# Kernel tuning notes

Hardware: AMD Instinct MI355X
Metric: run time of the kernel (lower is better)

Reference implementation:

```python
import jax, jax.numpy as jnp
import numpy as np

B, S, D = 1, 2048, 1024
H, HD = 16, 64            # attn_num, head dim (D = H*HD)
TE, K, ED = 16, 2, 512    # experts, top_k, expert_dim
DS = 2048                 # shared_expert_dim
EPS = 1e-5
THETA = 10000.0
RSF = 1.0                 # routed_scaling_factor


def rmsnorm(x, w):
    return x * jax.lax.rsqrt(jnp.mean(x * x, axis=-1, keepdims=True) + EPS) * w


def rope(x):
    # x: [B,H,S,a]; half-split rotary as in RotaryEmb
    a = x.shape[-1]
    inv = (1.0 / THETA) ** (jnp.arange(0, a, 2, dtype=jnp.float32) / a)
    fr = jnp.outer(jnp.arange(x.shape[2], dtype=jnp.float32), inv)[None, None]  # [1,1,S,a/2]
    c, s = jnp.cos(fr), jnp.sin(fr)
    x1, x2 = jnp.split(x, 2, axis=-1)
    return jnp.concatenate([x1 * c + x2 * s, -x1 * s + x2 * c], axis=-1)


def setup_inputs() -> dict:
    key = jax.random.key(0)
    ks = jax.random.split(key, 16)
    w = 0.02
    return {
        "x_input": jax.random.normal(ks[0], (B, S, D), jnp.float32),
        "indices": jax.random.randint(ks[1], (B * S, K), 0, TE),
        "values": jax.random.normal(ks[2], (B * S, K), jnp.float32),
        "attn_w": jax.random.normal(ks[3], (3 * D, D), jnp.float32) * w,
        "attn_o_w": jax.random.normal(ks[4], (D, D), jnp.float32) * w,
        "attn_norm_w": jnp.ones((D,), jnp.float32),
        "ffn_norm_w": jnp.ones((D,), jnp.float32),
        "ffn_experts": jax.random.normal(ks[5], (3, TE, D, ED), jnp.float32) * w,
        "main_keys": jax.random.normal(ks[6], (D, TE), jnp.float32) * w,
        "main_bias": jnp.zeros((TE,), jnp.float32),
        "output_coeff": jnp.ones((1, 1, D), jnp.float32),
        "ffn_up_w": jax.random.normal(ks[7], (2 * DS, D), jnp.float32) * w,
        "ffn_down_w": jax.random.normal(ks[8], (D, DS), jnp.float32) * w,
        "shared_norm_w": jnp.ones((D,), jnp.float32),
    }


def reference(x_input, indices, values, attn_w, attn_o_w, attn_norm_w, ffn_norm_w,
              ffn_experts, main_keys, main_bias, output_coeff, ffn_up_w,
              ffn_down_w, shared_norm_w):
    # --- attention block ---
    x = rmsnorm(x_input, attn_norm_w)
    qkv = x @ attn_w.T                                  # [B,S,3D]
    xq, xk, xv = jnp.split(qkv, 3, axis=-1)
    def heads(t):
        return t.reshape(B, S, H, HD).transpose(0, 2, 1, 3)  # [B,H,S,HD]
    q, k, v = rope(heads(xq)), rope(heads(xk)), heads(xv)
    att = jnp.einsum('bhqa,bhka->bhqk', q, k) / jnp.sqrt(jnp.float32(HD))
    causal = jnp.tril(jnp.ones((S, S), bool))
    att = jnp.where(causal, att, jnp.finfo(att.dtype).min)
    att = jax.nn.softmax(att, axis=-1)
    o = jnp.einsum('bhqk,bhka->bhqa', att, v)
    x_attn = o.transpose(0, 2, 1, 3).reshape(B, S, D)
    x_ffn_input = x_attn @ attn_o_w.T + x_input

    # --- router ---
    x_ffn = rmsnorm(x_ffn_input, ffn_norm_w)
    T = B * S
    token_values = (x_ffn @ main_keys).reshape(T, TE)
    tv = jnp.take_along_axis(token_values, indices, axis=-1)  # [T,K]
    vals = values + tv + main_bias[indices]
    scores = jax.nn.softmax(vals, axis=-1) * RSF              # [T,K]

    # --- grouped GEMM experts (SwiGLU), dense combine over experts ---
    combine = jnp.zeros((T, TE), x_ffn.dtype).at[
        jnp.arange(T)[:, None], indices].add(scores)          # [T,TE]
    xf = x_ffn.reshape(T, D)
    h1 = jnp.einsum('td,edh->eth', xf, ffn_experts[0])
    h2 = jnp.einsum('td,edh->eth', xf, ffn_experts[1])
    g = jax.nn.silu(h1) * h2                                  # [TE,T,ED]
    ye = jnp.einsum('eth,edh->etd', g, ffn_experts[2])        # [TE,T,D]
    y = jnp.einsum('etd,te->td', ye, combine).reshape(B, S, D)
    y = y * output_coeff

    # --- shared SwiGLU expert ---
    x1, x2 = jnp.split(x_ffn @ ffn_up_w.T, 2, axis=-1)
    y_shared = (jax.nn.silu(x1) * x2) @ ffn_down_w.T
    y_shared = rmsnorm(y_shared, shared_norm_w)

    return y + y_shared + x_ffn_input
```

## Files before the change

### kernel.cpp

```cpp
#include <hip/hip_runtime.h>
#include <hip/hip_bf16.h>

using bf16 = __hip_bfloat16;

#define S_   2048
#define D_   1024
#define H_   16
#define HD_  64
#define TE_  16
#define ED_  512
#define DS_  2048
#define CAP_ 512

#define NEG_ -1e30f

typedef __attribute__((ext_vector_type(8))) short bf16x8;
typedef __attribute__((ext_vector_type(4))) short bf16x4;
typedef __attribute__((ext_vector_type(4))) float f32x4;
#define MFMA16(a, b, c) __builtin_amdgcn_mfma_f32_16x16x32_bf16(a, b, c, 0, 0, 0)

__device__ __forceinline__ void storeF(float* p, float v) { *p = v; }
__device__ __forceinline__ void storeF(bf16* p, float v)  { *p = __float2bfloat16(v); }
__device__ __forceinline__ short cvt1(float f) {
    bf16 h = __float2bfloat16(f);
    return *(short*)&h;
}
__device__ __forceinline__ float b2f(short s) {
    return __uint_as_float(((unsigned)(unsigned short)s) << 16);
}

__device__ __forceinline__ void load16(const bf16* g, short* l) {
    __builtin_amdgcn_global_load_lds(
        (const __attribute__((address_space(1))) unsigned*)g,
        (__attribute__((address_space(3))) unsigned*)l, 16, 0, 0);
}

__global__ __launch_bounds__(256) void convert_kernel(
        const float* __restrict__ src, bf16* __restrict__ dst)
{
    const size_t i = ((size_t)blockIdx.x*256 + threadIdx.x)*8;
    const float4 f0 = *(const float4*)(src + i);
    const float4 f1 = *(const float4*)(src + i + 4);
    short t8[8];
    t8[0]=cvt1(f0.x); t8[1]=cvt1(f0.y); t8[2]=cvt1(f0.z); t8[3]=cvt1(f0.w);
    t8[4]=cvt1(f1.x); t8[5]=cvt1(f1.y); t8[6]=cvt1(f1.z); t8[7]=cvt1(f1.w);
    *(bf16x8*)(dst + i) = *(bf16x8*)t8;
}

__global__ __launch_bounds__(256) void mkT_kernel(
        const float* __restrict__ mk, float* __restrict__ mkT)
{
    const int idx = blockIdx.x*256 + threadIdx.x;
    const int e = idx >> 10, d = idx & 1023;
    mkT[idx] = mk[d*TE_ + e];
}

__global__ __launch_bounds__(256) void rmsnorm_kernel(
        const float* __restrict__ x, const float* __restrict__ w,
        bf16* __restrict__ out)
{
    const int t = blockIdx.x, tid = threadIdx.x;
    __shared__ float red[4];
    const float4 xv = *(const float4*)(x + (size_t)t*D_ + tid*4);
    float ss = xv.x*xv.x + xv.y*xv.y + xv.z*xv.z + xv.w*xv.w;
#pragma unroll
    for (int off = 32; off; off >>= 1) ss += __shfl_xor(ss, off, 64);
    if ((tid & 63) == 0) red[tid >> 6] = ss;
    __syncthreads();
    const float rn = rsqrtf((red[0]+red[1]+red[2]+red[3]) * (1.f/D_) + 1e-5f);
    const float4 wv = *(const float4*)(w + tid*4);
    short o[4];
    o[0] = cvt1(xv.x*rn*wv.x); o[1] = cvt1(xv.y*rn*wv.y);
    o[2] = cvt1(xv.z*rn*wv.z); o[3] = cvt1(xv.w*rn*wv.w);
    *(bf16x4*)(out + (size_t)t*D_ + tid*4) = *(bf16x4*)o;
}

template<typename OutT, bool HAS_RES, int BN>
__global__ __launch_bounds__(256) void gemm_mfma_bb_kernel(
    const bf16* __restrict__ A, const bf16* __restrict__ B,
    OutT* __restrict__ C, const float* __restrict__ Res,
    int M, int N, int K)
{
    constexpr int MI = (BN == 128) ? 4 : 2;
    __shared__ short As[2][128*32];
    __shared__ short Bs[2][BN*32];
    const int tid = threadIdx.x;
    const int w = tid >> 6, l = tid & 63;
    const int wm = (BN == 128) ? (w >> 1) : w;
    const int wn = (BN == 128) ? (w & 1) : 0;
    const int nwg = gridDim.x * gridDim.y;
    const int bid = blockIdx.y * gridDim.x + blockIdx.x;
    const int swz = ((nwg & 7) == 0) ? ((bid & 7) * (nwg >> 3) + (bid >> 3)) : bid;
    const int bx = swz % gridDim.x, by = swz / gridDim.x;
    const int m0 = by * 128, n0 = bx * BN;
    const int lr = l >> 2, lq = l & 3;
    const int fm = l & 15, fq = l >> 4;
    f32x4 acc[MI][4];
#pragma unroll
    for (int i = 0; i < MI; ++i)
#pragma unroll
        for (int j = 0; j < 4; ++j) acc[i][j] = (f32x4){0.f,0.f,0.f,0.f};

    const bf16* ga = A + (size_t)(m0 + w*16 + lr)*K + lq*8;
    const bf16* gb = B + (size_t)(n0 + w*16 + lr)*K + lq*8;
    load16(ga,                &As[0][(w*16)*32]);
    load16(ga + (size_t)64*K, &As[0][(64 + w*16)*32]);
    load16(gb,                &Bs[0][(w*16)*32]);
    if constexpr (BN == 128)
        load16(gb + (size_t)64*K, &Bs[0][(64 + w*16)*32]);
    __syncthreads();
    const int nk = K >> 5;
    for (int t = 0; t < nk; ++t) {
        const int cur = t & 1;
        if (t + 1 < nk) {
            const int k1 = (t + 1) << 5;
            load16(ga + k1,                &As[cur^1][(w*16)*32]);
            load16(ga + k1 + (size_t)64*K, &As[cur^1][(64 + w*16)*32]);
            load16(gb + k1,                &Bs[cur^1][(w*16)*32]);
            if constexpr (BN == 128)
                load16(gb + k1 + (size_t)64*K, &Bs[cur^1][(64 + w*16)*32]);
        }
        bf16x8 af[MI], bfr[4];
#pragma unroll
        for (int mi = 0; mi < MI; ++mi)
            af[mi] = *(const bf16x8*)&As[cur][(wm*(MI*16) + mi*16 + fm)*32 + fq*8];
#pragma unroll
        for (int ni = 0; ni < 4; ++ni)
            bfr[ni] = *(const bf16x8*)&Bs[cur][(wn*64 + ni*16 + fm)*32 + fq*8];
#pragma unroll
        for (int mi = 0; mi < MI; ++mi)
#pragma unroll
            for (int ni = 0; ni < 4; ++ni)
                acc[mi][ni] = MFMA16(af[mi], bfr[ni], acc[mi][ni]);
        __syncthreads();
    }
#pragma unroll
    for (int mi = 0; mi < MI; ++mi)
#pragma unroll
        for (int ni = 0; ni < 4; ++ni)
#pragma unroll
            for (int r = 0; r < 4; ++r) {
                const int row = m0 + wm*(MI*16) + mi*16 + fq*4 + r;
                const int col = n0 + wn*64 + ni*16 + fm;
                float v = acc[mi][ni][r];
                if constexpr (HAS_RES) v += Res[(size_t)row*N + col];
                storeF(&C[(size_t)row*N + col], v);
            }
}

__global__ __launch_bounds__(256) void transpose_kernel(
    const float* __restrict__ src, bf16* __restrict__ dst)
{
    __shared__ bf16 tile[64][65];
    const int h0 = blockIdx.x*64, d0 = blockIdx.y*64, m = blockIdx.z;
    const float* s = src + (size_t)m*D_*ED_;
    bf16*        o = dst + (size_t)m*ED_*D_;
    const int tid = threadIdx.x;
    const int r4 = tid >> 4, c4 = (tid & 15)*4;
#pragma unroll
    for (int i = 0; i < 4; ++i) {
        const int r = i*16 + r4;
        const float4 f = *(const float4*)&s[(size_t)(d0 + r)*ED_ + h0 + c4];
        tile[r][c4+0] = __float2bfloat16(f.x);
        tile[r][c4+1] = __float2bfloat16(f.y);
        tile[r][c4+2] = __float2bfloat16(f.z);
        tile[r][c4+3] = __float2bfloat16(f.w);
    }
    __syncthreads();
    const int hh8 = tid >> 3, cg = tid & 7;
#pragma unroll
    for (int j = 0; j < 2; ++j) {
        const int hh = j*32 + hh8;
        short t8[8];
#pragma unroll
        for (int e = 0; e < 8; ++e) t8[e] = *(short*)&tile[cg*8 + e][hh];
        *(bf16x8*)&o[(size_t)(h0 + hh)*D_ + d0 + cg*8] = *(bf16x8*)t8;
    }
}

__global__ __launch_bounds__(256) void expert_mid_mfma_kernel(
    const bf16* __restrict__ xffn, const bf16* __restrict__ w0t,
    const int* __restrict__ counts, const int* __restrict__ pairs,
    const float* __restrict__ pw, bf16* __restrict__ gbuf)
{
    const int ht = blockIdx.x, pt = blockIdx.y, e = blockIdx.z;
    const int cnt = counts[e];
    if (pt*128 >= cnt) return;
    __shared__ short Xs[2][128*32];
    __shared__ short W0s[2][64*32];
    __shared__ short W1s[2][64*32];
    __shared__ int   toks[128];
    __shared__ float wrow[128];
    const int tid = threadIdx.x;
    const int w = tid >> 6, l = tid & 63;
    const int wm = w >> 1, wn = w & 1;
    const int lr = l >> 2, lq = l & 3;
    const int fm = l & 15, fq = l >> 4;
    if (tid < 128) {
        const int p = pt*128 + tid;
        if (p < cnt) { toks[tid] = pairs[e*CAP_ + p] >> 1; wrow[tid] = pw[e*CAP_ + p]; }
        else         { toks[tid] = 0;                      wrow[tid] = 0.f; }
    }
    __syncthreads();
    const int t0 = toks[w*16 + lr], t1 = toks[64 + w*16 + lr];
    const bf16* gx0 = xffn + (size_t)t0*D_ + lq*8;
    const bf16* gx1 = xffn + (size_t)t1*D_ + lq*8;
    const bf16* g0  = w0t + ((size_t)e*ED_ + ht*64 + w*16 + lr)*D_ + lq*8;
    const bf16* g1  = w0t + ((size_t)(16 + e)*ED_ + ht*64 + w*16 + lr)*D_ + lq*8;
    f32x4 acc1[4][2], acc2[4][2];
#pragma unroll
    for (int i = 0; i < 4; ++i)
#pragma unroll
        for (int j = 0; j < 2; ++j) {
            acc1[i][j] = (f32x4){0.f,0.f,0.f,0.f};
            acc2[i][j] = (f32x4){0.f,0.f,0.f,0.f};
        }
    load16(gx0, &Xs[0][(w*16)*32]);
    load16(gx1, &Xs[0][(64 + w*16)*32]);
    load16(g0,  &W0s[0][(w*16)*32]);
    load16(g1,  &W1s[0][(w*16)*32]);
    __syncthreads();
    const int nk = D_ >> 5;
    for (int t = 0; t < nk; ++t) {
        const int cur = t & 1;
        if (t + 1 < nk) {
            const int k1 = (t + 1) << 5;
            load16(gx0 + k1, &Xs[cur^1][(w*16)*32]);
            load16(gx1 + k1, &Xs[cur^1][(64 + w*16)*32]);
            load16(g0 + k1,  &W0s[cur^1][(w*16)*32]);
            load16(g1 + k1,  &W1s[cur^1][(w*16)*32]);
        }
        bf16x8 af[4], b0[2], b1[2];
#pragma unroll
        for (int mi = 0; mi < 4; ++mi)
            af[mi] = *(const bf16x8*)&Xs[cur][(wm*64 + mi*16 + fm)*32 + fq*8];
#pragma unroll
        for (int ni = 0; ni < 2; ++ni) {
            b0[ni] = *(const bf16x8*)&W0s[cur][(wn*32 + ni*16 + fm)*32 + fq*8];
            b1[ni] = *(const bf16x8*)&W1s[cur][(wn*32 + ni*16 + fm)*32 + fq*8];
        }
#pragma unroll
        for (int mi = 0; mi < 4; ++mi)
#pragma unroll
            for (int ni = 0; ni < 2; ++ni) {
                acc1[mi][ni] = MFMA16(af[mi], b0[ni], acc1[mi][ni]);
                acc2[mi][ni] = MFMA16(af[mi], b1[ni], acc2[mi][ni]);
            }
        __syncthreads();
    }
#pragma unroll
    for (int mi = 0; mi < 4; ++mi)
#pragma unroll
        for (int ni = 0; ni < 2; ++ni)
#pragma unroll
            for (int r = 0; r < 4; ++r) {
                const int row = wm*64 + mi*16 + fq*4 + r;
                const int col = wn*32 + ni*16 + fm;
                const float h1 = acc1[mi][ni][r], h2 = acc2[mi][ni][r];
                const float g = wrow[row] * (h1 / (1.f + __expf(-h1))) * h2;
                gbuf[((size_t)e*CAP_ + pt*128 + row)*ED_ + ht*64 + col] = __float2bfloat16(g);
            }
}

__global__ __launch_bounds__(256) void shared_swiglu_kernel(
    const bf16* __restrict__ xffn, const bf16* __restrict__ upbf,
    bf16* __restrict__ gsh)
{
    const int nt = blockIdx.x, mt = blockIdx.y;
    __shared__ short Xs[2][128*32];
    __shared__ short W0s[2][64*32];
    __shared__ short W1s[2][64*32];
    const int tid = threadIdx.x;
    const int w = tid >> 6, l = tid & 63;
    const int wm = w >> 1, wn = w & 1;
    const int lr = l >> 2, lq = l & 3;
    const int fm = l & 15, fq = l >> 4;
    const int m0 = mt*128, n0 = nt*64;
    const bf16* gx0 = xffn + (size_t)(m0 + w*16 + lr)*D_ + lq*8;
    const bf16* gx1 = xffn + (size_t)(m0 + 64 + w*16 + lr)*D_ + lq*8;
    const bf16* g0  = upbf + (size_t)(n0 + w*16 + lr)*D_ + lq*8;
    const bf16* g1  = upbf + (size_t)(DS_ + n0 + w*16 + lr)*D_ + lq*8;
    f32x4 acc1[4][2], acc2[4][2];
#pragma unroll
    for (int i = 0; i < 4; ++i)
#pragma unroll
        for (int j = 0; j < 2; ++j) {
            acc1[i][j] = (f32x4){0.f,0.f,0.f,0.f};
            acc2[i][j] = (f32x4){0.f,0.f,0.f,0.f};
        }
    load16(gx0, &Xs[0][(w*16)*32]);
    load16(gx1, &Xs[0][(64 + w*16)*32]);
    load16(g0,  &W0s[0][(w*16)*32]);
    load16(g1,  &W1s[0][(w*16)*32]);
    __syncthreads();
    const int nk = D_ >> 5;
    for (int t = 0; t < nk; ++t) {
        const int cur = t & 1;
        if (t + 1 < nk) {
            const int k1 = (t + 1) << 5;
            load16(gx0 + k1, &Xs[cur^1][(w*16)*32]);
            load16(gx1 + k1, &Xs[cur^1][(64 + w*16)*32]);
            load16(g0 + k1,  &W0s[cur^1][(w*16)*32]);
            load16(g1 + k1,  &W1s[cur^1][(w*16)*32]);
        }
        bf16x8 af[4], b0[2], b1[2];
#pragma unroll
        for (int mi = 0; mi < 4; ++mi)
            af[mi] = *(const bf16x8*)&Xs[cur][(wm*64 + mi*16 + fm)*32 + fq*8];
#pragma unroll
        for (int ni = 0; ni < 2; ++ni) {
            b0[ni] = *(const bf16x8*)&W0s[cur][(wn*32 + ni*16 + fm)*32 + fq*8];
            b1[ni] = *(const bf16x8*)&W1s[cur][(wn*32 + ni*16 + fm)*32 + fq*8];
        }
#pragma unroll
        for (int mi = 0; mi < 4; ++mi)
#pragma unroll
            for (int ni = 0; ni < 2; ++ni) {
                acc1[mi][ni] = MFMA16(af[mi], b0[ni], acc1[mi][ni]);
                acc2[mi][ni] = MFMA16(af[mi], b1[ni], acc2[mi][ni]);
            }
        __syncthreads();
    }
#pragma unroll
    for (int mi = 0; mi < 4; ++mi)
#pragma unroll
        for (int ni = 0; ni < 2; ++ni)
#pragma unroll
            for (int r = 0; r < 4; ++r) {
                const int row = wm*64 + mi*16 + fq*4 + r;
                const int col = wn*32 + ni*16 + fm;
                const float h1 = acc1[mi][ni][r], h2 = acc2[mi][ni][r];
                const float g = (h1 / (1.f + __expf(-h1))) * h2;
                gsh[(size_t)(m0 + row)*DS_ + n0 + col] = __float2bfloat16(g);
            }
}

__global__ __launch_bounds__(256) void expert_down_mfma_kernel(
    const bf16* __restrict__ gbuf, const bf16* __restrict__ w2,
    const int* __restrict__ counts, const int* __restrict__ pairs,
    bf16* __restrict__ ytk)
{
    const int nt = blockIdx.x, pt = blockIdx.y, e = blockIdx.z;
    const int cnt = counts[e];
    if (pt*128 >= cnt) return;
    __shared__ short As[2][128*32];
    __shared__ short Bs[2][128*32];
    __shared__ int prs[128];
    const int tid = threadIdx.x;
    const int w = tid >> 6, l = tid & 63;
    const int wm = w >> 1, wn = w & 1;
    const int lr = l >> 2, lq = l & 3;
    const int fm = l & 15, fq = l >> 4;
    if (tid < 128) {
        const int p = pt*128 + tid;
        prs[tid] = (p < cnt) ? pairs[e*CAP_ + p] : -1;
    }
    __syncthreads();
    const bf16* ga = gbuf + ((size_t)e*CAP_ + pt*128 + w*16 + lr)*ED_ + lq*8;
    const bf16* gb = w2 + (size_t)e*D_*ED_ + (size_t)(nt*128 + w*16 + lr)*ED_ + lq*8;
    f32x4 acc[4][4];
#pragma unroll
    for (int i = 0; i < 4; ++i)
#pragma unroll
        for (int j = 0; j < 4; ++j) acc[i][j] = (f32x4){0.f,0.f,0.f,0.f};
    load16(ga,                  &As[0][(w*16)*32]);
    load16(ga + (size_t)64*ED_, &As[0][(64 + w*16)*32]);
    load16(gb,                  &Bs[0][(w*16)*32]);
    load16(gb + (size_t)64*ED_, &Bs[0][(64 + w*16)*32]);
    __syncthreads();
    const int nk = ED_ >> 5;
    for (int t = 0; t < nk; ++t) {
        const int cur = t & 1;
        if (t + 1 < nk) {
            const int k1 = (t + 1) << 5;
            load16(ga + k1,                  &As[cur^1][(w*16)*32]);
            load16(ga + k1 + (size_t)64*ED_, &As[cur^1][(64 + w*16)*32]);
            load16(gb + k1,                  &Bs[cur^1][(w*16)*32]);
            load16(gb + k1 + (size_t)64*ED_, &Bs[cur^1][(64 + w*16)*32]);
        }
        bf16x8 af[4], bfr[4];
#pragma unroll
        for (int mi = 0; mi < 4; ++mi)
            af[mi] = *(const bf16x8*)&As[cur][(wm*64 + mi*16 + fm)*32 + fq*8];
#pragma unroll
        for (int ni = 0; ni < 4; ++ni)
            bfr[ni] = *(const bf16x8*)&Bs[cur][(wn*64 + ni*16 + fm)*32 + fq*8];
#pragma unroll
        for (int mi = 0; mi < 4; ++mi)
#pragma unroll
            for (int ni = 0; ni < 4; ++ni)
                acc[mi][ni] = MFMA16(af[mi], bfr[ni], acc[mi][ni]);
        __syncthreads();
    }
#pragma unroll
    for (int mi = 0; mi < 4; ++mi)
#pragma unroll
        for (int r = 0; r < 4; ++r) {
            const int pr = prs[wm*64 + mi*16 + fq*4 + r];
            if (pr < 0) continue;
#pragma unroll
            for (int ni = 0; ni < 4; ++ni) {
                const int col = nt*128 + wn*64 + ni*16 + fm;
                ytk[(size_t)pr*D_ + col] = __float2bfloat16(acc[mi][ni][r]);
            }
        }
}

__global__ __launch_bounds__(256) void rope_kernel(const bf16* __restrict__ qkv,
        bf16* __restrict__ qr, bf16* __restrict__ kswz)
{
    const int s = blockIdx.x, tid = threadIdx.x;
    const int c = s & 63, jt = s >> 6;
    for (int it = tid; it < 512; it += 256) {
        const int h = it >> 5, i = it & 31;
        const float inv = exp2f(-(float)i * 0.41524101186091903f);
        const float fr = (float)s * inv;
        float sn, cs;
        sincosf(fr, &sn, &cs);
        const size_t qb = (size_t)s*3072 + h*64 + i;
        const float q1 = __bfloat162float(qkv[qb]);
        const float q2 = __bfloat162float(qkv[qb + 32]);
        const size_t ob = ((size_t)h*S_ + s)*64 + i;
        qr[ob]      = __float2bfloat16(0.125f*( q1*cs + q2*sn));
        qr[ob + 32] = __float2bfloat16(0.125f*(-q1*sn + q2*cs));
        const float k1 = __bfloat162float(qkv[qb + 1024]);
        const float k2 = __bfloat162float(qkv[qb + 1024 + 32]);
        const size_t kb = ((size_t)(h*32 + jt))*4096 + (size_t)c*64;
        const int j0 = (i >> 3) ^ (c & 7);
        const int j1 = (4 + (i >> 3)) ^ (c & 7);
        kswz[kb + j0*8 + (i & 7)] = __float2bfloat16( k1*cs + k2*sn);
        kswz[kb + j1*8 + (i & 7)] = __float2bfloat16(-k1*sn + k2*cs);
    }
}

__global__ __launch_bounds__(256) void vtrans_kernel(
    const bf16* __restrict__ qkv, bf16* __restrict__ vswz)
{
    const int jt = blockIdx.x, h = blockIdx.y;
    __shared__ short Vt[64][72];
    const int tid = threadIdx.x;
#pragma unroll
    for (int it = 0; it < 2; ++it) {
        const int idx = it*256 + tid;
        const int cc = idx >> 3, seg = idx & 7;
        *(bf16x8*)&Vt[cc][seg*8] =
            *(const bf16x8*)(qkv + (size_t)(jt*64 + cc)*3072 + 2048 + h*64 + seg*8);
    }
    __syncthreads();
    bf16* out = vswz + ((size_t)(h*32 + jt))*4096;
#pragma unroll
    for (int it = 0; it < 2; ++it) {
        const int q = it*256 + tid;
        const int a = q >> 3, jo = q & 7;
        const int j = jo ^ (a & 7);
        short t8[8];
#pragma unroll
        for (int e = 0; e < 8; ++e) t8[e] = Vt[j*8 + e][a];
        *(bf16x8*)(out + a*64 + jo*8) = *(bf16x8*)t8;
    }
}

__global__ __launch_bounds__(512) void attn_mfma_kernel(
    const bf16* __restrict__ qr, const bf16* __restrict__ kswz,
    const bf16* __restrict__ vswz, bf16* __restrict__ xattn)
{
    const int p = blockIdx.x, h = blockIdx.y;
    __shared__ short Ks[2][2][4096];
    __shared__ short Vs[2][2][4096];
    __shared__ short Ps[2][64][72];
    __shared__ float Oc[64][64];
    __shared__ float Mc[64], Lc[64];
    const int tid = threadIdx.x;
    const int w = tid >> 6, l = tid & 63;
    const int g = w >> 2, gw = w & 3;
    const int fm = l & 15, fq = l >> 4;
    const int sr = gw * 16;
    const bf16* ktile = kswz + (size_t)h*32*4096;
    const bf16* vtile = vswz + (size_t)h*32*4096;

    auto stageKV = [&](int jtile, int bufidx) {
        const bf16* ks_ = ktile + (size_t)jtile*4096 + gw*1024 + l*8;
        const bf16* vs_ = vtile + (size_t)jtile*4096 + gw*1024 + l*8;
        short* kd_ = &Ks[g][bufidx][gw*1024];
        short* vd_ = &Vs[g][bufidx][gw*1024];
        load16(ks_,       kd_);
        load16(ks_ + 512, kd_ + 512);
        load16(vs_,       vd_);
        load16(vs_ + 512, vd_ + 512);
    };

    for (int half = 0; half < 2; ++half) {
        const int qt = half ? (31 - p) : p;
        const bf16* gq = qr + ((size_t)h*S_ + qt*64 + sr + fm)*64 + fq*8;
        const bf16x8 aq0 = *(const bf16x8*)gq;
        const bf16x8 aq1 = *(const bf16x8*)(gq + 32);
        f32x4 Oa[4];
        float m_i[4], l_i[4];
#pragma unroll
        for (int i = 0; i < 4; ++i) {
            Oa[i] = (f32x4){0.f,0.f,0.f,0.f};
            m_i[i] = NEG_; l_i[i] = 0.f;
        }
        const int nj = qt + 1;
        const int itmax = (nj + 1) >> 1;
        if (g < nj) stageKV(g, 0);
        __syncthreads();
        for (int it = 0; it < itmax; ++it) {
            const int jt = g + 2*it;
            const int buf = it & 1;
            if (jt + 2 < nj) stageKV(jt + 2, buf ^ 1);
            if (jt < nj) {
                const short* kb = &Ks[g][buf][0];
                const short* vb = &Vs[g][buf][0];
                f32x4 sc[4];
#pragma unroll
                for (int ni = 0; ni < 4; ++ni) sc[ni] = (f32x4){0.f,0.f,0.f,0.f};
                __builtin_amdgcn_s_setprio(1);
#pragma unroll
                for (int ni = 0; ni < 4; ++ni) {
                    const int row = ni*16 + fm;
                    bf16x8 bk0 = *(const bf16x8*)&kb[row*64 + (( fq      ^ (fm & 7))<<3)];
                    bf16x8 bk1 = *(const bf16x8*)&kb[row*64 + (((fq + 4) ^ (fm & 7))<<3)];
                    sc[ni] = MFMA16(aq0, bk0, sc[ni]);
                    sc[ni] = MFMA16(aq1, bk1, sc[ni]);
                }
                __builtin_amdgcn_s_setprio(0);
                const bool diag = (jt == qt);
#pragma unroll
                for (int r = 0; r < 4; ++r) {
                    const int rowin = sr + fq*4 + r;
                    float rm = NEG_;
#pragma unroll
                    for (int ni = 0; ni < 4; ++ni) {
                        if (diag && (ni*16 + fm) > rowin) sc[ni][r] = NEG_;
                        rm = fmaxf(rm, sc[ni][r]);
                    }
                    rm = fmaxf(rm, __shfl_xor(rm, 1, 16));
                    rm = fmaxf(rm, __shfl_xor(rm, 2, 16));
                    rm = fmaxf(rm, __shfl_xor(rm, 4, 16));
                    rm = fmaxf(rm, __shfl_xor(rm, 8, 16));
                    const float mnew  = fmaxf(m_i[r], rm);
                    const float alpha = __expf(m_i[r] - mnew);
                    float rs = 0.f;
#pragma unroll
                    for (int ni = 0; ni < 4; ++ni) {
                        const float pv = __expf(sc[ni][r] - mnew);
                        sc[ni][r] = pv; rs += pv;
                    }
                    rs += __shfl_xor(rs, 1, 16);
                    rs += __shfl_xor(rs, 2, 16);
                    rs += __shfl_xor(rs, 4, 16);
                    rs += __shfl_xor(rs, 8, 16);
                    l_i[r] = l_i[r]*alpha + rs;
                    m_i[r] = mnew;
#pragma unroll
                    for (int ni = 0; ni < 4; ++ni) Oa[ni][r] *= alpha;
                }
#pragma unroll
                for (int ni = 0; ni < 4; ++ni)
#pragma unroll
                    for (int r = 0; r < 4; ++r)
                        Ps[g][sr + fq*4 + r][ni*16 + fm] = cvt1(sc[ni][r]);
                bf16x8 ap0 = *(const bf16x8*)&Ps[g][sr + fm][fq*8];
                bf16x8 ap1 = *(const bf16x8*)&Ps[g][sr + fm][32 + fq*8];
                __builtin_amdgcn_s_setprio(1);
#pragma unroll
                for (int ni = 0; ni < 4; ++ni) {
                    const int row = ni*16 + fm;
                    bf16x8 bv0 = *(const bf16x8*)&vb[row*64 + (( fq      ^ (fm & 7))<<3)];
                    bf16x8 bv1 = *(const bf16x8*)&vb[row*64 + (((fq + 4) ^ (fm & 7))<<3)];
                    Oa[ni] = MFMA16(ap0, bv0, Oa[ni]);
                    Oa[ni] = MFMA16(ap1, bv1, Oa[ni]);
                }
                __builtin_amdgcn_s_setprio(0);
            }
            __syncthreads();
        }
        if (g == 1) {
#pragma unroll
            for (int r = 0; r < 4; ++r) {
                const int row = sr + fq*4 + r;
                if (fm == 0) { Mc[row] = m_i[r]; Lc[row] = l_i[r]; }
#pragma unroll
                for (int ni = 0; ni < 4; ++ni) Oc[row][ni*16 + fm] = Oa[ni][r];
            }
        }
        __syncthreads();
        if (g == 0) {
#pragma unroll
            for (int r = 0; r < 4; ++r) {
                const int row = sr + fq*4 + r;
                const float m1 = Mc[row], l1 = Lc[row];
                const float mm = fmaxf(m_i[r], m1);
                const float a0 = __expf(m_i[r] - mm), a1 = __expf(m1 - mm);
                const float inv = 1.f / (l_i[r]*a0 + l1*a1);
                const int srow = qt*64 + row;
#pragma unroll
                for (int ni = 0; ni < 4; ++ni)
                    xattn[(size_t)srow*D_ + h*64 + ni*16 + fm] =
                        __float2bfloat16((Oa[ni][r]*a0 + Oc[row][ni*16 + fm]*a1)*inv);
            }
        }
        __syncthreads();
    }
}

__global__ __launch_bounds__(256) void router_kernel(
    const bf16* __restrict__ xffn, const int* __restrict__ indices,
    const float* __restrict__ values, const float* __restrict__ mkT,
    const float* __restrict__ mbias, int* __restrict__ counts,
    int* __restrict__ pairs, float* __restrict__ pw)
{
    const int wv = threadIdx.x >> 6, lane = threadIdx.x & 63;
    const int t = blockIdx.x*4 + wv;
    const int i0 = indices[t*2], i1 = indices[t*2 + 1];
    const bf16* xp = xffn + (size_t)t*D_ + lane*16;
    const bf16x8 xa = *(const bf16x8*)xp;
    const bf16x8 xb = *(const bf16x8*)(xp + 8);
    float xv[16];
#pragma unroll
    for (int j = 0; j < 8; ++j) { xv[j] = b2f(xa[j]); xv[8 + j] = b2f(xb[j]); }
    const float* k0 = mkT + (size_t)i0*D_ + lane*16;
    const float* k1 = mkT + (size_t)i1*D_ + lane*16;
    float a0[16], a1[16];
#pragma unroll
    for (int j = 0; j < 4; ++j) {
        *(float4*)&a0[j*4] = *(const float4*)(k0 + j*4);
        *(float4*)&a1[j*4] = *(const float4*)(k1 + j*4);
    }
    float s0 = 0.f, s1 = 0.f;
#pragma unroll
    for (int j = 0; j < 16; ++j) {
        s0 = fmaf(xv[j], a0[j], s0);
        s1 = fmaf(xv[j], a1[j], s1);
    }
#pragma unroll
    for (int off = 32; off; off >>= 1) {
        s0 += __shfl_xor(s0, off, 64);
        s1 += __shfl_xor(s1, off, 64);
    }
    if (lane == 0) {
        const float v0 = values[t*2]     + s0 + mbias[i0];
        const float v1 = values[t*2 + 1] + s1 + mbias[i1];
        const float mx = fmaxf(v0, v1);
        const float e0 = __expf(v0 - mx), e1 = __expf(v1 - mx);
        const float inv = 1.f / (e0 + e1);
        const int p0 = atomicAdd(&counts[i0], 1);
        if (p0 < CAP_) { pairs[i0*CAP_ + p0] = t*2;     pw[i0*CAP_ + p0] = e0*inv; }
        const int p1 = atomicAdd(&counts[i1], 1);
        if (p1 < CAP_) { pairs[i1*CAP_ + p1] = t*2 + 1; pw[i1*CAP_ + p1] = e1*inv; }
    }
}

__global__ __launch_bounds__(256) void final_kernel(
    const bf16* __restrict__ ytk, const float* __restrict__ ysh,
    const float* __restrict__ xffin, const float* __restrict__ coeff,
    const float* __restrict__ shw, float* __restrict__ out)
{
    const int t = blockIdx.x, tid = threadIdx.x;
    __shared__ float red[4];
    const float4 yv = *(const float4*)(ysh + (size_t)t*D_ + tid*4);
    float ss = yv.x*yv.x + yv.y*yv.y + yv.z*yv.z + yv.w*yv.w;
#pragma unroll
    for (int off = 32; off; off >>= 1) ss += __shfl_xor(ss, off, 64);
    if ((tid & 63) == 0) red[tid >> 6] = ss;
    __syncthreads();
    const float rn = rsqrtf((red[0]+red[1]+red[2]+red[3]) * (1.f/D_) + 1e-5f);
    const int d = tid*4;
    const bf16x4 y0 = *(const bf16x4*)(ytk + (size_t)(t*2)*D_ + d);
    const bf16x4 y1 = *(const bf16x4*)(ytk + (size_t)(t*2 + 1)*D_ + d);
    const float4 cf = *(const float4*)(coeff + d);
    const float4 sw = *(const float4*)(shw + d);
    const float4 xf = *(const float4*)(xffin + (size_t)t*D_ + d);
    float4 o;
    o.x = (b2f(y0[0]) + b2f(y1[0]))*cf.x + yv.x*rn*sw.x + xf.x;
    o.y = (b2f(y0[1]) + b2f(y1[1]))*cf.y + yv.y*rn*sw.y + xf.y;
    o.z = (b2f(y0[2]) + b2f(y1[2]))*cf.z + yv.z*rn*sw.z + xf.z;
    o.w = (b2f(y0[3]) + b2f(y1[3]))*cf.w + yv.w*rn*sw.w + xf.w;
    *(float4*)(out + (size_t)t*D_ + d) = o;
}

extern "C" void kernel_launch(void* const* d_in, const int* in_sizes, int n_in,
                              void* d_out, int out_size, void* d_ws, size_t ws_size,
                              hipStream_t stream)
{
    const float* x_input     = (const float*)d_in[0];
    const int*   indices     = (const int*)  d_in[1];
    const float* values      = (const float*)d_in[2];
    const float* attn_w      = (const float*)d_in[3];
    const float* attn_o_w    = (const float*)d_in[4];
    const float* attn_norm_w = (const float*)d_in[5];
    const float* ffn_norm_w  = (const float*)d_in[6];
    const float* ffn_experts = (const float*)d_in[7];
    const float* main_keys   = (const float*)d_in[8];
    const float* main_bias   = (const float*)d_in[9];
    const float* out_coeff   = (const float*)d_in[10];
    const float* ffn_up_w    = (const float*)d_in[11];
    const float* ffn_down_w  = (const float*)d_in[12];
    const float* shared_nw   = (const float*)d_in[13];

    char* wp = (char*)d_ws;
    auto alloc = [&](size_t n) { char* p = wp; wp += (n + 255) & ~(size_t)255; return p; };
    char*  regA   = alloc(28*1024*1024 + 4096);
    bf16*  xn     = (bf16*)(regA);
    bf16*  qkv    = (bf16*)(regA + 4*1024*1024);
    bf16*  qr     = (bf16*)(regA + 16*1024*1024);
    bf16*  xattn  = (bf16*)(regA + 20*1024*1024);
    bf16*  w2bf   = (bf16*)(regA);
    bf16*  gsh    = (bf16*)(regA + 16*1024*1024);
    float* xffin  = (float*)alloc((size_t)S_*D_*4);
    bf16*  kswz   = (bf16*)xffin;
    bf16*  vswz   = kswz + (size_t)H_*32*4096;
    bf16*  xffn   = (bf16*) alloc((size_t)S_*D_*2);
    int*   counts = (int*)  alloc(TE_*4);
    int*   pairs  = (int*)  alloc((size_t)TE_*CAP_*4);
    float* pwgt   = (float*)alloc((size_t)TE_*CAP_*4);
    float* mkT    = (float*)alloc((size_t)TE_*D_*4);
    bf16*  gbuf   = (bf16*) alloc((size_t)TE_*CAP_*ED_*2);
    bf16*  o_bf   = (bf16*)gbuf;
    float* ysh    = (float*)((char*)gbuf);
    bf16*  ytk    = (bf16*) alloc((size_t)S_*2*D_*2);
    bf16*  awbf   = (bf16*)ytk;
    bf16*  w0t    = (bf16*) alloc((size_t)2*TE_*ED_*D_*2);
    bf16*  upbf   = (bf16*)w0t;
    bf16*  dnbf   = (bf16*)((char*)w0t + 8*1024*1024);

    hipMemsetAsync(counts, 0, TE_*4, stream);

    convert_kernel<<<(3*D_*D_)/2048, 256, 0, stream>>>(attn_w, awbf);
    convert_kernel<<<(D_*D_)/2048, 256, 0, stream>>>(attn_o_w, o_bf);
    mkT_kernel<<<(TE_*D_)/256, 256, 0, stream>>>(main_keys, mkT);

    rmsnorm_kernel<<<S_, 256, 0, stream>>>(x_input, attn_norm_w, xn);
    gemm_mfma_bb_kernel<bf16,false,128><<<dim3(3*D_/128, S_/128), 256, 0, stream>>>(
        xn, awbf, qkv, nullptr, S_, 3*D_, D_);
    rope_kernel<<<S_, 256, 0, stream>>>(qkv, qr, kswz);
    vtrans_kernel<<<dim3(S_/64, H_), 256, 0, stream>>>(qkv, vswz);
    attn_mfma_kernel<<<dim3(16, H_), 512, 0, stream>>>(qr, kswz, vswz, xattn);

    transpose_kernel<<<dim3(ED_/64, D_/64, 2*TE_), 256, 0, stream>>>(ffn_experts, w0t);

    gemm_mfma_bb_kernel<float,true,64><<<dim3(D_/64, S_/128), 256, 0, stream>>>(
        xattn, o_bf, xffin, x_input, S_, D_, D_);

    rmsnorm_kernel<<<S_, 256, 0, stream>>>(xffin, ffn_norm_w, xffn);
    router_kernel<<<S_/4, 256, 0, stream>>>(xffn, indices, values, mkT, main_bias,
                                            counts, pairs, pwgt);
    convert_kernel<<<(TE_*D_*ED_)/2048, 256, 0, stream>>>(
        ffn_experts + (size_t)2*TE_*D_*ED_, w2bf);
    expert_mid_mfma_kernel<<<dim3(ED_/64, CAP_/128, TE_), 256, 0, stream>>>(
        xffn, w0t, counts, pairs, pwgt, gbuf);
    convert_kernel<<<(2*DS_*D_)/2048, 256, 0, stream>>>(ffn_up_w, upbf);
    convert_kernel<<<(D_*DS_)/2048, 256, 0, stream>>>(ffn_down_w, dnbf);

    shared_swiglu_kernel<<<dim3(DS_/64, S_/128), 256, 0, stream>>>(xffn, upbf, gsh);

    expert_down_mfma_kernel<<<dim3(D_/128, CAP_/128, TE_), 256, 0, stream>>>(
        gbuf, w2bf, counts, pairs, ytk);

    gemm_mfma_bb_kernel<float,false,64><<<dim3(D_/64, S_/128), 256, 0, stream>>>(
        gsh, dnbf, ysh, nullptr, S_, D_, DS_);

    final_kernel<<<S_, 256, 0, stream>>>(ytk, ysh, xffin, out_coeff, shared_nw,
                                         (float*)d_out);
}
```

Before: 489.6 us.

## Triple-buffer LDS in MFMA GEMM kernels with vmcnt-based waits and single barrier

Converts the double-buffered global-to-LDS pipelines in the dense GEMM, expert up/mid, shared-expert up and expert down kernels to a three-stage ring with a prefetch distance of two tiles. Each iteration waits only for the oldest outstanding loads via s_waitcnt vmcnt(N) plus one barrier, instead of the implicit full drain and trailing __syncthreads. The aim is to hide more global-load latency behind the MFMA work. The cost is 1.5x the LDS footprint, which may lower occupancy. The hand-counted vmcnt values depend on the exact number of loads issued per stage.

```diff
diff --git a/kernel.cpp b/kernel.cpp
--- a/kernel.cpp
+++ b/kernel.cpp
@@ -33,6 +33,22 @@
     __builtin_amdgcn_global_load_lds(
         (const __attribute__((address_space(1))) unsigned*)g,
         (__attribute__((address_space(3))) unsigned*)l, 16, 0, 0);
+}
+
+__device__ __forceinline__ void pipe_wait_vm4() {
+    asm volatile("s_waitcnt vmcnt(4)" ::: "memory");
+    __builtin_amdgcn_s_barrier();
+    __builtin_amdgcn_sched_barrier(0);
+}
+__device__ __forceinline__ void pipe_wait_vm3() {
+    asm volatile("s_waitcnt vmcnt(3)" ::: "memory");
+    __builtin_amdgcn_s_barrier();
+    __builtin_amdgcn_sched_barrier(0);
+}
+__device__ __forceinline__ void pipe_wait_vm0() {
+    asm volatile("s_waitcnt vmcnt(0)" ::: "memory");
+    __builtin_amdgcn_s_barrier();
+    __builtin_amdgcn_sched_barrier(0);
 }
 
 __global__ __launch_bounds__(256) void convert_kernel(
@@ -82,8 +98,8 @@
     int M, int N, int K)
 {
     constexpr int MI = (BN == 128) ? 4 : 2;
-    __shared__ short As[2][128*32];
-    __shared__ short Bs[2][BN*32];
+    __shared__ short As[3][128*32];
+    __shared__ short Bs[3][BN*32];
     const int tid = threadIdx.x;
     const int w = tid >> 6, l = tid & 63;
     const int wm = (BN == 128) ? (w >> 1) : w;
@@ -103,22 +119,27 @@
 
     const bf16* ga = A + (size_t)(m0 + w*16 + lr)*K + lq*8;
     const bf16* gb = B + (size_t)(n0 + w*16 + lr)*K + lq*8;
-    load16(ga,                &As[0][(w*16)*32]);
-    load16(ga + (size_t)64*K, &As[0][(64 + w*16)*32]);
-    load16(gb,                &Bs[0][(w*16)*32]);
-    if constexpr (BN == 128)
-        load16(gb + (size_t)64*K, &Bs[0][(64 + w*16)*32]);
-    __syncthreads();
+
+    auto stage = [&](int buf, int k0) {
+        load16(ga + k0,                &As[buf][(w*16)*32]);
+        load16(ga + k0 + (size_t)64*K, &As[buf][(64 + w*16)*32]);
+        load16(gb + k0,                &Bs[buf][(w*16)*32]);
+        if constexpr (BN == 128)
+            load16(gb + k0 + (size_t)64*K, &Bs[buf][(64 + w*16)*32]);
+    };
     const int nk = K >> 5;
+    stage(0, 0);
+    stage(1, 32);
+    int cur = 0;
     for (int t = 0; t < nk; ++t) {
-        const int cur = t & 1;
         if (t + 1 < nk) {
-            const int k1 = (t + 1) << 5;
-            load16(ga + k1,                &As[cur^1][(w*16)*32]);
-            load16(ga + k1 + (size_t)64*K, &As[cur^1][(64 + w*16)*32]);
-            load16(gb + k1,                &Bs[cur^1][(w*16)*32]);
-            if constexpr (BN == 128)
-                load16(gb + k1 + (size_t)64*K, &Bs[cur^1][(64 + w*16)*32]);
+            if constexpr (BN == 128) pipe_wait_vm4(); else pipe_wait_vm3();
+        } else {
+            pipe_wait_vm0();
+        }
+        if (t + 2 < nk) {
+            const int stg = (cur + 2 >= 3) ? cur - 1 : cur + 2;
+            stage(stg, (t + 2) << 5);
         }
         bf16x8 af[MI], bfr[4];
 #pragma unroll
@@ -132,7 +153,7 @@
 #pragma unroll
             for (int ni = 0; ni < 4; ++ni)
                 acc[mi][ni] = MFMA16(af[mi], bfr[ni], acc[mi][ni]);
-        __syncthreads();
+        cur = (cur == 2) ? 0 : cur + 1;
     }
 #pragma unroll
     for (int mi = 0; mi < MI; ++mi)
@@ -186,9 +207,9 @@
     const int ht = blockIdx.x, pt = blockIdx.y, e = blockIdx.z;
     const int cnt = counts[e];
     if (pt*128 >= cnt) return;
-    __shared__ short Xs[2][128*32];
-    __shared__ short W0s[2][64*32];
-    __shared__ short W1s[2][64*32];
+    __shared__ short Xs[3][128*32];
+    __shared__ short W0s[3][64*32];
+    __shared__ short W1s[3][64*32];
     __shared__ int   toks[128];
     __shared__ float wrow[128];
     const int tid = threadIdx.x;
@@ -215,20 +236,21 @@
             acc1[i][j] = (f32x4){0.f,0.f,0.f,0.f};
             acc2[i][j] = (f32x4){0.f,0.f,0.f,0.f};
         }
-    load16(gx0, &Xs[0][(w*16)*32]);
-    load16(gx1, &Xs[0][(64 + w*16)*32]);
-    load16(g0,  &W0s[0][(w*16)*32]);
-    load16(g1,  &W1s[0][(w*16)*32]);
-    __syncthreads();
+    auto stage = [&](int buf, int k0) {
+        load16(gx0 + k0, &Xs[buf][(w*16)*32]);
+        load16(gx1 + k0, &Xs[buf][(64 + w*16)*32]);
+        load16(g0 + k0,  &W0s[buf][(w*16)*32]);
+        load16(g1 + k0,  &W1s[buf][(w*16)*32]);
+    };
     const int nk = D_ >> 5;
+    stage(0, 0);
+    stage(1, 32);
+    int cur = 0;
     for (int t = 0; t < nk; ++t) {
-        const int cur = t & 1;
-        if (t + 1 < nk) {
-            const int k1 = (t + 1) << 5;
-            load16(gx0 + k1, &Xs[cur^1][(w*16)*32]);
-            load16(gx1 + k1, &Xs[cur^1][(64 + w*16)*32]);
-            load16(g0 + k1,  &W0s[cur^1][(w*16)*32]);
-            load16(g1 + k1,  &W1s[cur^1][(w*16)*32]);
+        if (t + 1 < nk) pipe_wait_vm4(); else pipe_wait_vm0();
+        if (t + 2 < nk) {
+            const int stg = (cur + 2 >= 3) ? cur - 1 : cur + 2;
+            stage(stg, (t + 2) << 5);
         }
         bf16x8 af[4], b0[2], b1[2];
 #pragma unroll
@@ -246,7 +268,7 @@
                 acc1[mi][ni] = MFMA16(af[mi], b0[ni], acc1[mi][ni]);
                 acc2[mi][ni] = MFMA16(af[mi], b1[ni], acc2[mi][ni]);
             }
-        __syncthreads();
+        cur = (cur == 2) ? 0 : cur + 1;
     }
 #pragma unroll
     for (int mi = 0; mi < 4; ++mi)
@@ -267,9 +289,9 @@
     bf16* __restrict__ gsh)
 {
     const int nt = blockIdx.x, mt = blockIdx.y;
-    __shared__ short Xs[2][128*32];
-    __shared__ short W0s[2][64*32];
-    __shared__ short W1s[2][64*32];
+    __shared__ short Xs[3][128*32];
+    __shared__ short W0s[3][64*32];
+    __shared__ short W1s[3][64*32];
     const int tid = threadIdx.x;
     const int w = tid >> 6, l = tid & 63;
     const int wm = w >> 1, wn = w & 1;
@@ -288,20 +310,21 @@
             acc1[i][j] = (f32x4){0.f,0.f,0.f,0.f};
             acc2[i][j] = (f32x4){0.f,0.f,0.f,0.f};
         }
-    load16(gx0, &Xs[0][(w*16)*32]);
-    load16(gx1, &Xs[0][(64 + w*16)*32]);
-    load16(g0,  &W0s[0][(w*16)*32]);
-    load16(g1,  &W1s[0][(w*16)*32]);
-    __syncthreads();
+    auto stage = [&](int buf, int k0) {
+        load16(gx0 + k0, &Xs[buf][(w*16)*32]);
+        load16(gx1 + k0, &Xs[buf][(64 + w*16)*32]);
+        load16(g0 + k0,  &W0s[buf][(w*16)*32]);
+        load16(g1 + k0,  &W1s[buf][(w*16)*32]);
+    };
     const int nk = D_ >> 5;
+    stage(0, 0);
+    stage(1, 32);
+    int cur = 0;
     for (int t = 0; t < nk; ++t) {
-        const int cur = t & 1;
-        if (t + 1 < nk) {
-            const int k1 = (t + 1) << 5;
-            load16(gx0 + k1, &Xs[cur^1][(w*16)*32]);
-            load16(gx1 + k1, &Xs[cur^1][(64 + w*16)*32]);
-            load16(g0 + k1,  &W0s[cur^1][(w*16)*32]);
-            load16(g1 + k1,  &W1s[cur^1][(w*16)*32]);
+        if (t + 1 < nk) pipe_wait_vm4(); else pipe_wait_vm0();
+        if (t + 2 < nk) {
+            const int stg = (cur + 2 >= 3) ? cur - 1 : cur + 2;
+            stage(stg, (t + 2) << 5);
         }
         bf16x8 af[4], b0[2], b1[2];
 #pragma unroll
@@ -319,7 +342,7 @@
                 acc1[mi][ni] = MFMA16(af[mi], b0[ni], acc1[mi][ni]);
                 acc2[mi][ni] = MFMA16(af[mi], b1[ni], acc2[mi][ni]);
             }
-        __syncthreads();
+        cur = (cur == 2) ? 0 : cur + 1;
     }
 #pragma unroll
     for (int mi = 0; mi < 4; ++mi)
@@ -343,8 +366,8 @@
     const int nt = blockIdx.x, pt = blockIdx.y, e = blockIdx.z;
     const int cnt = counts[e];
     if (pt*128 >= cnt) return;
-    __shared__ short As[2][128*32];
-    __shared__ short Bs[2][128*32];
+    __shared__ short As[3][128*32];
+    __shared__ short Bs[3][128*32];
     __shared__ int prs[128];
     const int tid = threadIdx.x;
     const int w = tid >> 6, l = tid & 63;
@@ -363,20 +386,21 @@
     for (int i = 0; i < 4; ++i)
 #pragma unroll
         for (int j = 0; j < 4; ++j) acc[i][j] = (f32x4){0.f,0.f,0.f,0.f};
-    load16(ga,                  &As[0][(w*16)*32]);
-    load16(ga + (size_t)64*ED_, &As[0][(64 + w*16)*32]);
-    load16(gb,                  &Bs[0][(w*16)*32]);
-    load16(gb + (size_t)64*ED_, &Bs[0][(64 + w*16)*32]);
-    __syncthreads();
+    auto stage = [&](int buf, int k0) {
+        load16(ga + k0,                  &As[buf][(w*16)*32]);
+        load16(ga + k0 + (size_t)64*ED_, &As[buf][(64 + w*16)*32]);
+        load16(gb + k0,                  &Bs[buf][(w*16)*32]);
+        load16(gb + k0 + (size_t)64*ED_, &Bs[buf][(64 + w*16)*32]);
+    };
     const int nk = ED_ >> 5;
+    stage(0, 0);
+    stage(1, 32);
+    int cur = 0;
     for (int t = 0; t < nk; ++t) {
-        const int cur = t & 1;
-        if (t + 1 < nk) {
-            const int k1 = (t + 1) << 5;
-            load16(ga + k1,                  &As[cur^1][(w*16)*32]);
-            load16(ga + k1 + (size_t)64*ED_, &As[cur^1][(64 + w*16)*32]);
-            load16(gb + k1,                  &Bs[cur^1][(w*16)*32]);
-            load16(gb + k1 + (size_t)64*ED_, &Bs[cur^1][(64 + w*16)*32]);
+        if (t + 1 < nk) pipe_wait_vm4(); else pipe_wait_vm0();
+        if (t + 2 < nk) {
+            const int stg = (cur + 2 >= 3) ? cur - 1 : cur + 2;
+            stage(stg, (t + 2) << 5);
         }
         bf16x8 af[4], bfr[4];
 #pragma unroll
@@ -390,7 +414,7 @@
 #pragma unroll
             for (int ni = 0; ni < 4; ++ni)
                 acc[mi][ni] = MFMA16(af[mi], bfr[ni], acc[mi][ni]);
-        __syncthreads();
+        cur = (cur == 2) ? 0 : cur + 1;
     }
 #pragma unroll
     for (int mi = 0; mi < 4; ++mi)
```

After: 492.0 us. Within noise of the previous version (+0.5%).
